# Kernel tuning notes

Hardware: AMD Instinct MI355X
Metric: run time of the kernel (lower is better)

The kernel has to match this reference:

```python
import jax, jax.numpy as jnp
import numpy as np
from jax import lax

EPOCHS = 3
N_IN, N_OUT = 20, 18
BN_EPS = 1e-5
RECT_EPS = 1e-4
TRIU = np.triu_indices(N_OUT)  # SPDVectorize upper-triangular indices


def _orth(key, n, m):
    # Stiefel init: orthonormal columns, like nn.init.orthogonal_
    q, _ = jnp.linalg.qr(jax.random.normal(key, (n, m), dtype=jnp.float32))
    return q


def setup_inputs() -> dict:
    key = jax.random.key(0)
    ks = jax.random.split(key, 8)
    bs = 2048
    f32 = jnp.float32
    return dict(
        x=jax.random.normal(ks[0], (bs, 1, 22, 438), dtype=f32),
        W1=jax.random.normal(ks[1], (22, 1, 22, 1), dtype=f32) * 0.1,
        b1=jnp.zeros((22,), f32),
        g1=jnp.ones((22,), f32), be1=jnp.zeros((22,), f32),
        W2=jax.random.normal(ks[2], (20, 22, 1, 12), dtype=f32) * 0.05,
        b2=jnp.zeros((20,), f32),
        g2=jnp.ones((20,), f32), be2=jnp.zeros((20,), f32),
        Wq=_orth(ks[3], N_IN, N_OUT),
        Wk=_orth(ks[4], N_IN, N_OUT),
        Wv=_orth(ks[5], N_IN, N_OUT),
        Wl=jax.random.normal(ks[6], (N_OUT * (N_OUT + 1) // 2 * EPOCHS, 4), dtype=f32) * 0.02,
        bl=jnp.zeros((4,), f32),
    )


def _bn(x, g, b):
    # BatchNorm2d forward in training mode (batch statistics, biased var)
    mean = x.mean(axis=(0, 2, 3), keepdims=True)
    var = ((x - mean) ** 2).mean(axis=(0, 2, 3), keepdims=True)
    return (x - mean) * lax.rsqrt(var + BN_EPS) * g[None, :, None, None] + b[None, :, None, None]


def _conv(x, w, b, pad_w):
    y = lax.conv_general_dilated(x, w, (1, 1), [(0, 0), (pad_w, pad_w)],
                                 dimension_numbers=('NCHW', 'OIHW', 'NCHW'))
    return y + b[None, :, None, None]


def _signal2spd(x):
    # x: (bs, C, L) -> trace-normalized covariance + 1e-5 * I
    L = x.shape[-1]
    xc = x - x.mean(-1, keepdims=True)
    cov = jnp.einsum('bcl,bdl->bcd', xc, xc) / (L - 1)
    cov = cov / jnp.trace(cov, axis1=-2, axis2=-1)[:, None, None]
    return cov + 1e-5 * jnp.eye(cov.shape[-1], dtype=cov.dtype)


def _patch_lens(n, epochs):
    base = n // epochs
    lens = [base] * epochs
    for i in range(n - base * epochs):
        lens[i] += 1
    return lens


def _spd_fn(t, fn):
    # SPD functional calculus via eigh (== torch.svd on SPD input)
    s, u = jnp.linalg.eigh(t)
    return jnp.einsum('...ij,...j,...kj->...ik', u, fn(s), u)


def _forward(x, W1, b1, g1, be1, W2, b2, g2, be2, Wq, Wk, Wv, Wl, bl):
    bs = x.shape[0]
    h = _bn(_conv(x, W1, b1, 0), g1, be1)          # (bs,22,1,438)
    h = _bn(_conv(h, W2, b2, 6), g2, be2)          # (bs,20,1,439)
    sig = h[:, :, 0, :]                            # squeeze -> (bs,20,439)
    covs, off = [], 0
    for L in _patch_lens(sig.shape[-1], EPOCHS):   # E2R: [147,146,146]
        covs.append(_signal2spd(sig[:, :, off:off + L]))
        off += L
    X = jnp.stack(covs, axis=1)                    # (bs,m,20,20) SPD
    # SPDTransform: W^T X W with Stiefel W (20,18)
    Q = jnp.einsum('pi,bmpq,qj->bmij', Wq, X, Wq)
    K = jnp.einsum('pi,bmpq,qj->bmij', Wk, X, Wk)
    V = jnp.einsum('pi,bmpq,qj->bmij', Wv, X, Wv)
    logQ = _spd_fn(Q, jnp.log)
    logK = _spd_fn(K, jnp.log)
    logV = _spd_fn(V, jnp.log)
    # log-Euclidean distance^2: ||log Q_j - log K_i||_F^2  (== sum of svd singvals of D D^T)
    diff = logQ[:, :, None] - logK[:, None, :]     # (bs, mq, mk, n, n)
    energy = jnp.sum(diff * diff, axis=(-2, -1))   # (bs, mq, mk)
    scores = 1.0 / (1.0 + jnp.log1p(energy))
    # torch: softmax over dim=-2 then permute(0,2,1) == softmax over K index here
    P = jax.nn.softmax(scores, axis=-1)            # (bs, mq, mk)
    mixed = jnp.einsum('bji,bipq->bjpq', P, logV)  # weighted log-Euclidean mean
    out = _spd_fn(mixed, jnp.exp)
    out = _spd_fn(out, lambda s: jnp.maximum(s, RECT_EPS))  # SPDRectified
    logO = _spd_fn(out, jnp.log)                   # SPDTangentSpace log
    vec = logO[..., TRIU[0], TRIU[1]]              # (bs, m, 171)
    return vec.reshape(bs, -1) @ Wl + bl           # (bs, 4)


def reference(x, W1, b1, g1, be1, W2, b2, g2, be2, Wq, Wk, Wv, Wl, bl):
    return _forward(x, W1, b1, g1, be1, W2, b2, g2, be2, Wq, Wk, Wv, Wl, bl)
```

## Files before the change

### kernel.cpp

```cpp
#include <hip/hip_runtime.h>
#include <math.h>

#define OFF_G3   0
#define OFF_QKV  17981440
#define OFF_ST   (17981440 + 5971968)
#define ST_SX   0
#define ST_SXX  22
#define ST_WF   506
#define ST_BF   990
#define ST_Y2S  1012
#define ST_Y2Q  1032
#define ST_TOT  1052

#define LOGEPS -9.210340371976182f
#define NSWEEP 5
#define SHIFT  12.0f

__global__ __launch_bounds__(256) void k0_zero(float* __restrict__ st){
  for (int i = threadIdx.x; i < ST_TOT; i += 256) st[i] = 0.f;
}

__global__ __launch_bounds__(256) void k1_xstats(const float* __restrict__ x, float* __restrict__ st){
  __shared__ __align__(16) float xs[22*444];
  const float* xb = x + (size_t)blockIdx.x * (22*438);
  for (int i = threadIdx.x; i < 22*444; i += 256){
    int h = i / 444, w = i - h*444;
    xs[i] = (w < 438) ? xb[h*438 + w] : 0.f;
  }
  __syncthreads();
  for (int t = threadIdx.x; t < 275; t += 256){
    if (t < 22){
      const float4* r = (const float4*)&xs[t*444];
      float4 acc = {0.f,0.f,0.f,0.f};
      for (int w = 0; w < 111; ++w){ float4 v = r[w]; acc.x+=v.x; acc.y+=v.y; acc.z+=v.z; acc.w+=v.w; }
      atomicAdd(&st[ST_SX + t], acc.x+acc.y+acc.z+acc.w);
    } else {
      int rem = t - 22, h = 0;
      while (rem >= 22 - h){ rem -= 22 - h; ++h; }
      int h2 = h + rem;
      const float4* ra = (const float4*)&xs[h*444];
      const float4* rb = (const float4*)&xs[h2*444];
      float4 acc = {0.f,0.f,0.f,0.f};
      for (int w = 0; w < 111; ++w){
        float4 a = ra[w], b = rb[w];
        acc.x = fmaf(a.x,b.x,acc.x); acc.y = fmaf(a.y,b.y,acc.y);
        acc.z = fmaf(a.z,b.z,acc.z); acc.w = fmaf(a.w,b.w,acc.w);
      }
      atomicAdd(&st[ST_SXX + h*22 + h2], acc.x+acc.y+acc.z+acc.w);
    }
  }
}

__global__ __launch_bounds__(64) void k1b_fold(const float* __restrict__ W1, const float* __restrict__ g1,
                                               const float* __restrict__ be1, float* __restrict__ st){
  int c = threadIdx.x;
  if (c >= 22) return;
  const float invN = 1.f / (2048.f*438.f);
  float mcol[22];
  float mu0 = 0.f;
  for (int h = 0; h < 22; ++h){ mcol[h] = W1[c*22 + h]; mu0 = fmaf(mcol[h], st[ST_SX + h], mu0); }
  mu0 *= invN;
  float qf = 0.f;
  for (int h = 0; h < 22; ++h)
    for (int h2 = h; h2 < 22; ++h2){
      float w = mcol[h]*mcol[h2]*st[ST_SXX + h*22 + h2];
      qf += (h2 == h) ? w : 2.f*w;
    }
  qf *= invN;
  float var = qf - mu0*mu0;
  float a1 = g1[c] * rsqrtf(var + 1e-5f);
  for (int h = 0; h < 22; ++h) st[ST_WF + h*22 + c] = a1 * mcol[h];
  st[ST_BF + c] = be1[c] - a1 * mu0;
}

__global__ __launch_bounds__(256) void k2_weff(const float* __restrict__ W2, const float* __restrict__ st,
                                               float* __restrict__ weff2, float* __restrict__ pfx){
  __shared__ float wf[484];
  __shared__ float bf[22];
  for (int i = threadIdx.x; i < 484; i += 256) wf[i] = st[ST_WF + i];
  if (threadIdx.x < 22) bf[threadIdx.x] = st[ST_BF + threadIdx.x];
  __syncthreads();
  for (int i = threadIdx.x; i < 5280; i += 256){
    int t = i % 12; int tmp = i / 12;
    int dl = tmp % 5; tmp /= 5;
    int h = tmp % 22; int dg = tmp / 22;
    int d = dg*5 + dl;
    float a = 0.f;
    for (int c = 0; c < 22; ++c) a = fmaf(W2[d*264 + c*12 + t], wf[h*22 + c], a);
    weff2[i] = a;
  }
  if (threadIdx.x < 20){
    int d = threadIdx.x;
    float run = 0.f;
    pfx[d*13 + 0] = 0.f;
    for (int t = 0; t < 12; ++t){
      float a = 0.f;
      for (int c = 0; c < 22; ++c) a = fmaf(W2[d*264 + c*12 + t], bf[c], a);
      run += a;
      pfx[d*13 + t + 1] = run;
    }
  }
}

__global__ __launch_bounds__(512, 3) void k3_convg(const float* __restrict__ x,
    const float* __restrict__ weff2, const float* __restrict__ pfx,
    float* __restrict__ st, float* __restrict__ g3o){
  __shared__ __align__(16) float smem[10304];
  float* ps   = smem + 9944;
  float* sloc = smem + 10204;
  float* qloc = smem + 10224;
  float* mus  = smem + 10244;
  int tid = threadIdx.x;
  int n = blockIdx.x;
  const float* xb = x + (size_t)n*9636;
  for (int i = tid; i < 22*452; i += 512){
    int h = i / 452, w = i - h*452;
    int gx = w - 6;
    smem[i] = (gx >= 0 && gx < 438) ? xb[h*438 + gx] : 0.f;
  }
  if (tid < 260) ps[tid] = pfx[tid];
  if (tid < 40){ if (tid < 20) sloc[tid] = 0.f; else qloc[tid-20] = 0.f; }
  __syncthreads();
  int wave = tid >> 6;
  int dg = __builtin_amdgcn_readfirstlane(wave >> 1);
  int ct = tid & 127;
  bool act = ct < 110;
  int c0 = act ? ct*4 : 0;
  float acc[5][4];
  #pragma unroll
  for (int dl = 0; dl < 5; ++dl)
    #pragma unroll
    for (int j = 0; j < 4; ++j) acc[dl][j] = 0.f;
  const float* wb = weff2 + dg*1320;
  #pragma unroll 1
  for (int h = 0; h < 22; ++h){
    const float4* xr = (const float4*)&smem[h*452 + c0];
    float4 v0 = xr[0], v1 = xr[1], v2 = xr[2], v3 = xr[3];
    float xw[16] = {v0.x,v0.y,v0.z,v0.w, v1.x,v1.y,v1.z,v1.w,
                    v2.x,v2.y,v2.z,v2.w, v3.x,v3.y,v3.z,v3.w};
    const float* wp = wb + h*60;
    #pragma unroll
    for (int dl = 0; dl < 5; ++dl){
      #pragma unroll
      for (int t = 0; t < 12; ++t){
        float w = wp[dl*12 + t];
        #pragma unroll
        for (int j = 0; j < 4; ++j)
          acc[dl][j] = fmaf(w, xw[t+j], acc[dl][j]);
      }
    }
  }
  float s5[5], q5[5];
  #pragma unroll
  for (int dl = 0; dl < 5; ++dl){ s5[dl] = 0.f; q5[dl] = 0.f; }
  if (act){
    #pragma unroll
    for (int dl = 0; dl < 5; ++dl){
      int d = dg*5 + dl;
      #pragma unroll
      for (int j = 0; j < 4; ++j){
        int gw = c0 + j;
        if (gw < 439){
          int lo = 6 - gw; if (lo < 0) lo = 0;
          int hi = 444 - gw; if (hi > 12) hi = 12;
          float val = acc[dl][j] + (ps[d*13 + hi] - ps[d*13 + lo]);
          acc[dl][j] = val;
          s5[dl] += val; q5[dl] = fmaf(val, val, q5[dl]);
        }
      }
    }
  }
  #pragma unroll
  for (int off = 32; off; off >>= 1){
    #pragma unroll
    for (int dl = 0; dl < 5; ++dl){
      s5[dl] += __shfl_down(s5[dl], off);
      q5[dl] += __shfl_down(q5[dl], off);
    }
  }
  if ((tid & 63) == 0){
    #pragma unroll
    for (int dl = 0; dl < 5; ++dl){
      atomicAdd(&sloc[dg*5 + dl], s5[dl]);
      atomicAdd(&qloc[dg*5 + dl], q5[dl]);
    }
  }
  __syncthreads();
  if (tid < 20){
    atomicAdd(&st[ST_Y2S + tid], sloc[tid]);
    atomicAdd(&st[ST_Y2Q + tid], qloc[tid]);
  }
  if (act){
    #pragma unroll
    for (int dl = 0; dl < 5; ++dl){
      int d = dg*5 + dl;
      #pragma unroll
      for (int j = 0; j < 4; ++j){
        int gw = c0 + j;
        if (gw < 439){
          int m = (gw >= 293) ? 2 : ((gw >= 147) ? 1 : 0);
          int lw = gw - ((m == 2) ? 293 : ((m == 1) ? 147 : 0));
          smem[m*2960 + d*148 + lw] = acc[dl][j];
        }
      }
    }
  }
  if (tid < 100){
    int d = tid/5, k = tid - d*5;
    int m = (k == 0) ? 0 : ((k < 3) ? 1 : 2);
    int lw = (k == 0) ? 147 : ((k == 1 || k == 3) ? 146 : 147);
    smem[m*2960 + d*148 + lw] = 0.f;
  }
  __syncthreads();
  if (tid < 60){
    int m = tid/20, d = tid - m*20;
    const float4* r = (const float4*)&smem[m*2960 + d*148];
    float4 a4 = {0.f,0.f,0.f,0.f};
    #pragma unroll 1
    for (int w = 0; w < 37; ++w){ float4 v = r[w]; a4.x+=v.x; a4.y+=v.y; a4.z+=v.z; a4.w+=v.w; }
    mus[tid] = a4.x+a4.y+a4.z+a4.w;
  }
  __syncthreads();
  for (int it = tid; it < 630; it += 512){
    int m = it/210, t = it - m*210;
    int rem = t, c = 0;
    while (rem >= 20 - c){ rem -= 20 - c; ++c; }
    int d = c + rem;
    const float4* ra = (const float4*)&smem[m*2960 + c*148];
    const float4* rb = (const float4*)&smem[m*2960 + d*148];
    float4 acc4 = {0.f,0.f,0.f,0.f};
    #pragma unroll 1
    for (int w = 0; w < 37; ++w){
      float4 a = ra[w], b = rb[w];
      acc4.x = fmaf(a.x,b.x,acc4.x); acc4.y = fmaf(a.y,b.y,acc4.y);
      acc4.z = fmaf(a.z,b.z,acc4.z); acc4.w = fmaf(a.w,b.w,acc4.w);
    }
    float invL = (m == 0) ? (1.f/147.f) : (1.f/146.f);
    float a = (acc4.x+acc4.y+acc4.z+acc4.w) - mus[m*20+c]*mus[m*20+d]*invL;
    float* gm = g3o + (size_t)n*1200 + m*400;
    gm[c*20 + d] = a; gm[d*20 + c] = a;
  }
}

__global__ __launch_bounds__(256) void k4_qkv(const float* __restrict__ g3i, const float* __restrict__ st,
    const float* __restrict__ g2, const float* __restrict__ Wq, const float* __restrict__ Wk,
    const float* __restrict__ Wv, float* __restrict__ qkv){
  __shared__ __align__(16) float G3[3][400];
  __shared__ float a2s[20];
  __shared__ __align__(16) float Bt[3][18][20];
  __shared__ __align__(16) float Tmt[3][360];
  __shared__ float rtr3[3];
  int tid = threadIdx.x, n = blockIdx.x;
  if (tid < 20){
    const float invN = 1.f/(2048.f*439.f);
    float s = st[ST_Y2S + tid]*invN;
    float q = st[ST_Y2Q + tid]*invN;
    a2s[tid] = g2[tid] * rsqrtf(q - s*s + 1e-5f);
  }
  const float* gi = g3i + (size_t)n*1200;
  for (int i = tid; i < 1200; i += 256) (&G3[0][0])[i] = gi[i];
  __syncthreads();
  for (int i = tid; i < 1080; i += 256){
    int wt = i/360, r = i - wt*360; int d = r/18, jj = r - d*18;
    const float* Wm = (wt==0) ? Wq : ((wt==1) ? Wk : Wv);
    Bt[wt][jj][d] = a2s[d]*Wm[d*18 + jj];
  }
  __syncthreads();
  for (int wt = 0; wt < 3; ++wt){
    for (int i = tid; i < 1083; i += 256){
      if (i < 1080){
        int m = i/360, r = i - m*360; int p = r/18, jj = r - p*18;
        const float4* gr = (const float4*)&G3[m][p*20];
        const float4* br = (const float4*)&Bt[wt][jj][0];
        float4 a4 = {0.f,0.f,0.f,0.f};
        #pragma unroll
        for (int w = 0; w < 5; ++w){
          float4 a = gr[w], b = br[w];
          a4.x = fmaf(a.x,b.x,a4.x); a4.y = fmaf(a.y,b.y,a4.y);
          a4.z = fmaf(a.z,b.z,a4.z); a4.w = fmaf(a.w,b.w,a4.w);
        }
        Tmt[m][jj*20 + p] = a4.x+a4.y+a4.z+a4.w;
      } else if (wt == 0){
        int m = i - 1080;
        float tr = 0.f;
        for (int c = 0; c < 20; ++c){ float a = a2s[c]; tr = fmaf(a*a, G3[m][c*21], tr); }
        rtr3[m] = 1.f/tr;
      }
    }
    __syncthreads();
    for (int it = tid; it < 513; it += 256){
      int m = it/171, t = it - m*171;
      int rem = t, i = 0;
      while (rem >= 18 - i){ rem -= 18 - i; ++i; }
      int jj = i + rem;
      const float4* br = (const float4*)&Bt[wt][i][0];
      const float4* tr = (const float4*)&Tmt[m][jj*20];
      float4 a4 = {0.f,0.f,0.f,0.f};
      #pragma unroll
      for (int w = 0; w < 5; ++w){
        float4 a = br[w], b = tr[w];
        a4.x = fmaf(a.x,b.x,a4.x); a4.y = fmaf(a.y,b.y,a4.y);
        a4.z = fmaf(a.z,b.z,a4.z); a4.w = fmaf(a.w,b.w,a4.w);
      }
      float acc = (a4.x+a4.y+a4.z+a4.w) * rtr3[m];
      if (i == jj) acc += 1e-5f;
      float* outm = qkv + ((size_t)wt*6144 + (size_t)n*3 + m)*324;
      outm[i*18 + jj] = acc; outm[jj*18 + i] = acc;
    }
    __syncthreads();
  }
}

__global__ __launch_bounds__(256, 4) void k5_oneside(const float* __restrict__ src, float* __restrict__ dst,
    int nmat, int mode, const float* __restrict__ Wl, const float* __restrict__ bl,
    float* __restrict__ outp){
  __shared__ __align__(16) float stage[12][384];
  __shared__ __align__(16) float wls[2052];
  __shared__ float outacc[4][4];
  int tid = threadIdx.x;
  int wave = tid >> 6, lane = tid & 63;
  int g = (lane >= 54) ? 3 : (lane >= 36 ? 2 : (lane >= 18 ? 1 : 0));
  int j = lane - g*18;
  int gb = g*18;
  int slot = wave*3 + ((g < 3) ? g : 0);
  int mat = blockIdx.x*12 + wave*3 + g;
  bool act = (g < 3) && (mat < nmat);

  if (mode == 1){
    for (int i = tid; i < 2052; i += 256) wls[i] = Wl[i];
    if (tid < 16) outacc[tid >> 2][tid & 3] = 0.f;
  }

  float b[18];
  float sh = (mode == 1) ? SHIFT : 0.f;
  if (act){
    const float* s = src + (size_t)mat*324 + j*18;
    #pragma unroll
    for (int i = 0; i < 18; ++i) b[i] = s[i] + ((i == j) ? sh : 0.f);
  } else {
    #pragma unroll
    for (int i = 0; i < 18; ++i) b[i] = (i == j) ? 1.f : 0.f;
  }
  float nrm;
  { float n0 = 0.f, n1 = 0.f;
    #pragma unroll
    for (int k = 0; k < 18; k += 2){ n0 = fmaf(b[k],b[k],n0); n1 = fmaf(b[k+1],b[k+1],n1); }
    nrm = n0 + n1; }

  #pragma unroll 1
  for (int sweep = 0; sweep < NSWEEP; ++sweep){
    #pragma unroll
    for (int r = 0; r < 17; ++r){
      int xx = j - 1 - r; if (xx < 0) xx += 17;
      int v = r + 17 - xx; if (v >= 17) v -= 17;
      int m = (j == 0) ? (1 + r) : ((xx == 0) ? 0 : (1 + v));
      bool isp = (j == 0) ? true : ((xx == 0) ? false : (xx <= 8));
      int plane = (gb + m) & 63;
      float rv[18];
      #pragma unroll
      for (int k = 0; k < 18; ++k) rv[k] = __shfl(b[k], plane);
      float on = __shfl(nrm, plane);
      float g0 = 0.f, g1 = 0.f;
      #pragma unroll
      for (int k = 0; k < 18; k += 2){ g0 = fmaf(b[k], rv[k], g0); g1 = fmaf(b[k+1], rv[k+1], g1); }
      float gam = g0 + g1;
      float alpha = isp ? nrm : on;
      float beta  = isp ? on  : nrm;
      float tau = (beta - alpha) * 0.5f * __builtin_amdgcn_rcpf(gam);
      float tt = __builtin_amdgcn_rcpf(fabsf(tau) + sqrtf(fmaf(tau, tau, 1.f)));
      float t = (tau >= 0.f) ? tt : -tt;
      if (!(fabsf(gam) > 1e-36f)) t = 0.f;
      float c = __builtin_amdgcn_rsqf(fmaf(t, t, 1.f));
      float s = t*c;
      nrm = fmaf(isp ? -t : t, gam, nrm);
      float sg = isp ? -s : s;
      #pragma unroll
      for (int k = 0; k < 18; ++k) b[k] = fmaf(c, b[k], sg*rv[k]);
    }
  }
  float n0 = 0.f, n1 = 0.f;
  #pragma unroll
  for (int k = 0; k < 18; k += 2){ n0 = fmaf(b[k],b[k],n0); n1 = fmaf(b[k+1],b[k+1],n1); }
  float nf = fmaxf(n0 + n1, 1e-30f);
  float fv = (mode == 0) ? (0.5f * logf(nf)) : fmaxf(sqrtf(nf) - SHIFT, LOGEPS);
  float wv = fv * __builtin_amdgcn_rcpf(nf);
  float* sp = &stage[slot][0];
  if (act){
    #pragma unroll
    for (int k = 0; k < 18; ++k) sp[k*20 + j] = b[k];
    sp[360 + j] = wv;
  }
  __syncthreads();
  if (act){
    float wr[18];
    #pragma unroll
    for (int i = 0; i < 18; ++i) wr[i] = sp[j*20 + i] * sp[360 + i];
    float frow[18];
    #pragma unroll
    for (int i2 = 0; i2 < 18; ++i2){
      const float* br = &sp[i2*20];
      float a0 = 0.f;
      #pragma unroll
      for (int k = 0; k < 16; k += 4){
        float4 v4 = *(const float4*)&br[k];
        a0 = fmaf(wr[k],   v4.x, a0); a0 = fmaf(wr[k+1], v4.y, a0);
        a0 = fmaf(wr[k+2], v4.z, a0); a0 = fmaf(wr[k+3], v4.w, a0);
      }
      a0 = fmaf(wr[16], br[16], a0);
      a0 = fmaf(wr[17], br[17], a0);
      frow[i2] = a0;
    }
    if (mode == 0){
      float* orow = dst + (size_t)mat*324 + j*18;
      #pragma unroll
      for (int i2 = 0; i2 < 18; ++i2) orow[i2] = frow[i2];
    } else {
      int base = (g*171 + j*(37 - j)/2 - j)*4;
      float o0=0.f, o1=0.f, o2=0.f, o3=0.f;
      #pragma unroll
      for (int jj = 0; jj < 18; ++jj){
        if (jj >= j){
          const float* w4 = &wls[base + jj*4];
          o0 = fmaf(frow[jj], w4[0], o0);
          o1 = fmaf(frow[jj], w4[1], o1);
          o2 = fmaf(frow[jj], w4[2], o2);
          o3 = fmaf(frow[jj], w4[3], o3);
        }
      }
      atomicAdd(&outacc[wave][0], o0);
      atomicAdd(&outacc[wave][1], o1);
      atomicAdd(&outacc[wave][2], o2);
      atomicAdd(&outacc[wave][3], o3);
    }
  }
  if (mode == 1){
    __syncthreads();
    if (tid < 16){
      int bi = tid >> 2, o = tid & 3;
      outp[(blockIdx.x*4 + bi)*4 + o] = outacc[bi][o] + bl[o];
    }
  }
}

__global__ __launch_bounds__(128) void k6_attnmix(const float* __restrict__ logs, float* __restrict__ mixed){
  __shared__ float lq[972], lk[972], lv[972];
  __shared__ float ew[2][9];
  __shared__ float P[9];
  int b = blockIdx.x, tid = threadIdx.x;
  const float* q  = logs + (size_t)b*972;
  const float* k_ = logs + 1990656 + (size_t)b*972;
  const float* v_ = logs + 3981312 + (size_t)b*972;
  for (int i = tid; i < 972; i += 128){ lq[i] = q[i]; lk[i] = k_[i]; lv[i] = v_[i]; }
  __syncthreads();
  float e[9] = {0.f,0.f,0.f,0.f,0.f,0.f,0.f,0.f,0.f};
  for (int x = tid; x < 324; x += 128){
    float q0 = lq[x], q1 = lq[324+x], q2 = lq[648+x];
    float k0 = lk[x], k1 = lk[324+x], k2 = lk[648+x];
    float d;
    d = q0-k0; e[0] = fmaf(d,d,e[0]);
    d = q0-k1; e[1] = fmaf(d,d,e[1]);
    d = q0-k2; e[2] = fmaf(d,d,e[2]);
    d = q1-k0; e[3] = fmaf(d,d,e[3]);
    d = q1-k1; e[4] = fmaf(d,d,e[4]);
    d = q1-k2; e[5] = fmaf(d,d,e[5]);
    d = q2-k0; e[6] = fmaf(d,d,e[6]);
    d = q2-k1; e[7] = fmaf(d,d,e[7]);
    d = q2-k2; e[8] = fmaf(d,d,e[8]);
  }
  #pragma unroll
  for (int p = 0; p < 9; ++p)
    for (int off = 32; off; off >>= 1) e[p] += __shfl_down(e[p], off);
  if ((tid & 63) == 0){
    #pragma unroll
    for (int p = 0; p < 9; ++p) ew[tid >> 6][p] = e[p];
  }
  __syncthreads();
  if (tid < 3){
    float en0 = ew[0][tid*3+0] + ew[1][tid*3+0];
    float en1 = ew[0][tid*3+1] + ew[1][tid*3+1];
    float en2 = ew[0][tid*3+2] + ew[1][tid*3+2];
    float s0 = 1.f/(1.f + log1pf(en0));
    float s1 = 1.f/(1.f + log1pf(en1));
    float s2 = 1.f/(1.f + log1pf(en2));
    float mx = fmaxf(s0, fmaxf(s1, s2));
    float e0 = expf(s0-mx), e1 = expf(s1-mx), e2 = expf(s2-mx);
    float inv = 1.f/(e0+e1+e2);
    P[tid*3+0] = e0*inv; P[tid*3+1] = e1*inv; P[tid*3+2] = e2*inv;
  }
  __syncthreads();
  float p00=P[0],p01=P[1],p02=P[2],p10=P[3],p11=P[4],p12=P[5],p20=P[6],p21=P[7],p22=P[8];
  float* mb = mixed + (size_t)b*972;
  for (int x = tid; x < 324; x += 128){
    float v0 = lv[x], v1 = lv[324+x], v2 = lv[648+x];
    mb[x]     = p00*v0 + p01*v1 + p02*v2;
    mb[324+x] = p10*v0 + p11*v1 + p12*v2;
    mb[648+x] = p20*v0 + p21*v1 + p22*v2;
  }
}

extern "C" void kernel_launch(void* const* d_in, const int* in_sizes, int n_in,
                              void* d_out, int out_size, void* d_ws, size_t ws_size,
                              hipStream_t stream){
  (void)in_sizes; (void)n_in; (void)out_size; (void)ws_size;
  const float* x   = (const float*)d_in[0];
  const float* W1  = (const float*)d_in[1];
  const float* g1  = (const float*)d_in[3];
  const float* be1 = (const float*)d_in[4];
  const float* W2  = (const float*)d_in[5];
  const float* g2  = (const float*)d_in[7];
  const float* Wq  = (const float*)d_in[9];
  const float* Wk  = (const float*)d_in[10];
  const float* Wv  = (const float*)d_in[11];
  const float* Wl  = (const float*)d_in[12];
  const float* bl  = (const float*)d_in[13];
  float* ws    = (float*)d_ws;
  float* g3buf = ws + OFF_G3;
  float* qkv   = ws + OFF_QKV;
  float* weff2 = ws + OFF_QKV;
  float* pfx   = ws + OFF_QKV + 5280;
  float* logs  = ws + OFF_G3;
  float* mixed = ws + OFF_QKV;
  float* st    = ws + OFF_ST;
  float* outp  = (float*)d_out;

  k0_zero    <<<dim3(1),       dim3(256), 0, stream>>>(st);
  k1_xstats  <<<dim3(2048),    dim3(256), 0, stream>>>(x, st);
  k1b_fold   <<<dim3(1),       dim3(64),  0, stream>>>(W1, g1, be1, st);
  k2_weff    <<<dim3(1),       dim3(256), 0, stream>>>(W2, st, weff2, pfx);
  k3_convg   <<<dim3(2048),    dim3(512), 0, stream>>>(x, weff2, pfx, st, g3buf);
  k4_qkv     <<<dim3(2048),    dim3(256), 0, stream>>>(g3buf, st, g2, Wq, Wk, Wv, qkv);
  k5_oneside <<<dim3(1536),    dim3(256), 0, stream>>>(qkv, logs, 18432, 0, nullptr, nullptr, nullptr);
  k6_attnmix <<<dim3(2048),    dim3(128), 0, stream>>>(logs, mixed);
  k5_oneside <<<dim3(512),     dim3(256), 0, stream>>>(mixed, nullptr, 6144, 1, Wl, bl, outp);
}
```

Baseline: 695.3 us.

## Fuse QKV projection, eigen-log and attention mix into one per-sample kernel

Merges the QKV bilinear projection, the Jacobi eigendecomposition log of the Q/K/V matrices, and the attention energy/softmax/mix into one kernel per batch sample. The 18x18 matrices stay in shared memory, so the QKV and log buffers are no longer written to and read back from global memory and two launches go away. The Jacobi sweep loop is factored into a shared device function reused by the output-stage kernel. The conv kernel also reads the prefix table straight from global memory rather than staging it in LDS, and its launch bound is raised to 8 to allow more occupancy, which may raise register pressure or cause spills.

```diff
diff --git a/kernel.cpp b/kernel.cpp
--- a/kernel.cpp
+++ b/kernel.cpp
@@ -102,14 +102,13 @@
   }
 }
 
-__global__ __launch_bounds__(512, 3) void k3_convg(const float* __restrict__ x,
+__global__ __launch_bounds__(512, 8) void k3_convg(const float* __restrict__ x,
     const float* __restrict__ weff2, const float* __restrict__ pfx,
     float* __restrict__ st, float* __restrict__ g3o){
-  __shared__ __align__(16) float smem[10304];
-  float* ps   = smem + 9944;
-  float* sloc = smem + 10204;
-  float* qloc = smem + 10224;
-  float* mus  = smem + 10244;
+  __shared__ __align__(16) float smem[10044];
+  float* sloc = smem + 9944;
+  float* qloc = smem + 9964;
+  float* mus  = smem + 9984;
   int tid = threadIdx.x;
   int n = blockIdx.x;
   const float* xb = x + (size_t)n*9636;
@@ -118,7 +117,6 @@
     int gx = w - 6;
     smem[i] = (gx >= 0 && gx < 438) ? xb[h*438 + gx] : 0.f;
   }
-  if (tid < 260) ps[tid] = pfx[tid];
   if (tid < 40){ if (tid < 20) sloc[tid] = 0.f; else qloc[tid-20] = 0.f; }
   __syncthreads();
   int wave = tid >> 6;
@@ -157,13 +155,14 @@
     #pragma unroll
     for (int dl = 0; dl < 5; ++dl){
       int d = dg*5 + dl;
+      const float* prd = pfx + d*13;
       #pragma unroll
       for (int j = 0; j < 4; ++j){
         int gw = c0 + j;
         if (gw < 439){
           int lo = 6 - gw; if (lo < 0) lo = 0;
           int hi = 444 - gw; if (hi > 12) hi = 12;
-          float val = acc[dl][j] + (ps[d*13 + hi] - ps[d*13 + lo]);
+          float val = acc[dl][j] + (prd[hi] - prd[lo]);
           acc[dl][j] = val;
           s5[dl] += val; q5[dl] = fmaf(val, val, q5[dl]);
         }
@@ -242,15 +241,56 @@
   }
 }
 
-__global__ __launch_bounds__(256) void k4_qkv(const float* __restrict__ g3i, const float* __restrict__ st,
-    const float* __restrict__ g2, const float* __restrict__ Wq, const float* __restrict__ Wk,
-    const float* __restrict__ Wv, float* __restrict__ qkv){
-  __shared__ __align__(16) float G3[3][400];
+__device__ __forceinline__ void jacobi_sweeps(float b[18], float& nrm, int j, int gb){
+  #pragma unroll 1
+  for (int sweep = 0; sweep < NSWEEP; ++sweep){
+    #pragma unroll
+    for (int r = 0; r < 17; ++r){
+      int xx = j - 1 - r; if (xx < 0) xx += 17;
+      int v = r + 17 - xx; if (v >= 17) v -= 17;
+      int m = (j == 0) ? (1 + r) : ((xx == 0) ? 0 : (1 + v));
+      bool isp = (j == 0) ? true : ((xx == 0) ? false : (xx <= 8));
+      int plane = (gb + m) & 63;
+      float rv[18];
+      #pragma unroll
+      for (int k = 0; k < 18; ++k) rv[k] = __shfl(b[k], plane);
+      float on = __shfl(nrm, plane);
+      float g0 = 0.f, g1 = 0.f;
+      #pragma unroll
+      for (int k = 0; k < 18; k += 2){ g0 = fmaf(b[k], rv[k], g0); g1 = fmaf(b[k+1], rv[k+1], g1); }
+      float gam = g0 + g1;
+      float alpha = isp ? nrm : on;
+      float beta  = isp ? on  : nrm;
+      float tau = (beta - alpha) * 0.5f * __builtin_amdgcn_rcpf(gam);
+      float tt = __builtin_amdgcn_rcpf(fabsf(tau) + sqrtf(fmaf(tau, tau, 1.f)));
+      float t = (tau >= 0.f) ? tt : -tt;
+      if (!(fabsf(gam) > 1e-36f)) t = 0.f;
+      float c = __builtin_amdgcn_rsqf(fmaf(t, t, 1.f));
+      float s = t*c;
+      nrm = fmaf(isp ? -t : t, gam, nrm);
+      float sg = isp ? -s : s;
+      #pragma unroll
+      for (int k = 0; k < 18; ++k) b[k] = fmaf(c, b[k], sg*rv[k]);
+    }
+  }
+}
+
+__global__ __launch_bounds__(192, 6) void k5_mega(const float* __restrict__ g3i,
+    const float* __restrict__ st, const float* __restrict__ g2,
+    const float* __restrict__ Wq, const float* __restrict__ Wk, const float* __restrict__ Wv,
+    float* __restrict__ mixedo){
+  __shared__ __align__(16) float S[3420];
+  __shared__ __align__(16) float L[1539];
   __shared__ float a2s[20];
-  __shared__ __align__(16) float Bt[3][18][20];
-  __shared__ __align__(16) float Tmt[3][360];
   __shared__ float rtr3[3];
+  __shared__ float ew[3][9];
+  __shared__ float P[9];
   int tid = threadIdx.x, n = blockIdx.x;
+  int wave = tid >> 6, lane = tid & 63;
+
+  float* G3s = S;
+  float* Bt  = S + 1200;
+  float* Tmt = S + 2280;
   if (tid < 20){
     const float invN = 1.f/(2048.f*439.f);
     float s = st[ST_Y2S + tid]*invN;
@@ -258,20 +298,20 @@
     a2s[tid] = g2[tid] * rsqrtf(q - s*s + 1e-5f);
   }
   const float* gi = g3i + (size_t)n*1200;
-  for (int i = tid; i < 1200; i += 256) (&G3[0][0])[i] = gi[i];
-  __syncthreads();
-  for (int i = tid; i < 1080; i += 256){
+  for (int i = tid; i < 1200; i += 192) G3s[i] = gi[i];
+  __syncthreads();
+  for (int i = tid; i < 1080; i += 192){
     int wt = i/360, r = i - wt*360; int d = r/18, jj = r - d*18;
     const float* Wm = (wt==0) ? Wq : ((wt==1) ? Wk : Wv);
-    Bt[wt][jj][d] = a2s[d]*Wm[d*18 + jj];
+    Bt[wt*360 + jj*20 + d] = a2s[d]*Wm[d*18 + jj];
   }
   __syncthreads();
   for (int wt = 0; wt < 3; ++wt){
-    for (int i = tid; i < 1083; i += 256){
+    for (int i = tid; i < 1083; i += 192){
       if (i < 1080){
         int m = i/360, r = i - m*360; int p = r/18, jj = r - p*18;
-        const float4* gr = (const float4*)&G3[m][p*20];
-        const float4* br = (const float4*)&Bt[wt][jj][0];
+        const float4* gr = (const float4*)&G3s[m*400 + p*20];
+        const float4* br = (const float4*)&Bt[wt*360 + jj*20];
         float4 a4 = {0.f,0.f,0.f,0.f};
         #pragma unroll
         for (int w = 0; w < 5; ++w){
@@ -279,22 +319,22 @@
           a4.x = fmaf(a.x,b.x,a4.x); a4.y = fmaf(a.y,b.y,a4.y);
           a4.z = fmaf(a.z,b.z,a4.z); a4.w = fmaf(a.w,b.w,a4.w);
         }
-        Tmt[m][jj*20 + p] = a4.x+a4.y+a4.z+a4.w;
+        Tmt[m*360 + jj*20 + p] = a4.x+a4.y+a4.z+a4.w;
       } else if (wt == 0){
         int m = i - 1080;
         float tr = 0.f;
-        for (int c = 0; c < 20; ++c){ float a = a2s[c]; tr = fmaf(a*a, G3[m][c*21], tr); }
+        for (int c = 0; c < 20; ++c){ float a = a2s[c]; tr = fmaf(a*a, G3s[m*400 + c*21], tr); }
         rtr3[m] = 1.f/tr;
       }
     }
     __syncthreads();
-    for (int it = tid; it < 513; it += 256){
+    for (int it = tid; it < 513; it += 192){
       int m = it/171, t = it - m*171;
       int rem = t, i = 0;
       while (rem >= 18 - i){ rem -= 18 - i; ++i; }
       int jj = i + rem;
-      const float4* br = (const float4*)&Bt[wt][i][0];
-      const float4* tr = (const float4*)&Tmt[m][jj*20];
+      const float4* br = (const float4*)&Bt[wt*360 + i*20];
+      const float4* tr = (const float4*)&Tmt[m*360 + jj*20];
       float4 a4 = {0.f,0.f,0.f,0.f};
       #pragma unroll
       for (int w = 0; w < 5; ++w){
@@ -304,10 +344,122 @@
       }
       float acc = (a4.x+a4.y+a4.z+a4.w) * rtr3[m];
       if (i == jj) acc += 1e-5f;
-      float* outm = qkv + ((size_t)wt*6144 + (size_t)n*3 + m)*324;
-      outm[i*18 + jj] = acc; outm[jj*18 + i] = acc;
+      L[(wt*3 + m)*171 + i*(35-i)/2 + jj] = acc;
     }
     __syncthreads();
+  }
+
+  int g = (lane >= 54) ? 3 : (lane >= 36 ? 2 : (lane >= 18 ? 1 : 0));
+  int j = lane - g*18;
+  int gb = g*18;
+  int slot = wave*3 + ((g < 3) ? g : 0);
+  bool act = (g < 3);
+  float b[18];
+  if (act){
+    const float* mt = &L[(wave*3 + g)*171];
+    #pragma unroll
+    for (int i = 0; i < 18; ++i){
+      int r = (i < j) ? i : j;
+      int c = (i < j) ? j : i;
+      b[i] = mt[r*(35-r)/2 + c];
+    }
+  } else {
+    #pragma unroll
+    for (int i = 0; i < 18; ++i) b[i] = (i == j) ? 1.f : 0.f;
+  }
+  float nrm;
+  { float n0 = 0.f, n1 = 0.f;
+    #pragma unroll
+    for (int k = 0; k < 18; k += 2){ n0 = fmaf(b[k],b[k],n0); n1 = fmaf(b[k+1],b[k+1],n1); }
+    nrm = n0 + n1; }
+  jacobi_sweeps(b, nrm, j, gb);
+  { float n0 = 0.f, n1 = 0.f;
+    #pragma unroll
+    for (int k = 0; k < 18; k += 2){ n0 = fmaf(b[k],b[k],n0); n1 = fmaf(b[k+1],b[k+1],n1); }
+    float nf = fmaxf(n0 + n1, 1e-30f);
+    float fv = 0.5f * logf(nf);
+    float wv = fv * __builtin_amdgcn_rcpf(nf);
+    float* sp = &S[slot*380];
+    if (act){
+      #pragma unroll
+      for (int k = 0; k < 18; ++k) sp[k*20 + j] = b[k];
+      sp[360 + j] = wv;
+    }
+    __syncthreads();
+    if (act){
+      float wr[18];
+      #pragma unroll
+      for (int i = 0; i < 18; ++i) wr[i] = sp[j*20 + i] * sp[360 + i];
+      float frow[18];
+      #pragma unroll
+      for (int i2 = 0; i2 < 18; ++i2){
+        const float* br = &sp[i2*20];
+        float a0 = 0.f;
+        #pragma unroll
+        for (int k = 0; k < 16; k += 4){
+          float4 v4 = *(const float4*)&br[k];
+          a0 = fmaf(wr[k],   v4.x, a0); a0 = fmaf(wr[k+1], v4.y, a0);
+          a0 = fmaf(wr[k+2], v4.z, a0); a0 = fmaf(wr[k+3], v4.w, a0);
+        }
+        a0 = fmaf(wr[16], br[16], a0);
+        a0 = fmaf(wr[17], br[17], a0);
+        frow[i2] = a0;
+      }
+      float* orow = &S[wave*1140 + g*324 + j*18];
+      #pragma unroll
+      for (int i2 = 0; i2 < 18; ++i2) orow[i2] = frow[i2];
+    }
+  }
+  __syncthreads();
+
+  const float* lq = &S[0];
+  const float* lk = &S[1140];
+  const float* lv = &S[2280];
+  float e[9] = {0.f,0.f,0.f,0.f,0.f,0.f,0.f,0.f,0.f};
+  for (int x = tid; x < 324; x += 192){
+    float q0 = lq[x], q1 = lq[324+x], q2 = lq[648+x];
+    float k0 = lk[x], k1 = lk[324+x], k2 = lk[648+x];
+    float d;
+    d = q0-k0; e[0] = fmaf(d,d,e[0]);
+    d = q0-k1; e[1] = fmaf(d,d,e[1]);
+    d = q0-k2; e[2] = fmaf(d,d,e[2]);
+    d = q1-k0; e[3] = fmaf(d,d,e[3]);
+    d = q1-k1; e[4] = fmaf(d,d,e[4]);
+    d = q1-k2; e[5] = fmaf(d,d,e[5]);
+    d = q2-k0; e[6] = fmaf(d,d,e[6]);
+    d = q2-k1; e[7] = fmaf(d,d,e[7]);
+    d = q2-k2; e[8] = fmaf(d,d,e[8]);
+  }
+  #pragma unroll
+  for (int p = 0; p < 9; ++p)
+    for (int off = 32; off; off >>= 1) e[p] += __shfl_down(e[p], off);
+  if (lane == 0){
+    #pragma unroll
+    for (int p = 0; p < 9; ++p) ew[wave][p] = e[p];
+  }
+  __syncthreads();
+  if (tid < 3){
+    float en0 = ew[0][tid*3+0] + ew[1][tid*3+0] + ew[2][tid*3+0];
+    float en1 = ew[0][tid*3+1] + ew[1][tid*3+1] + ew[2][tid*3+1];
+    float en2 = ew[0][tid*3+2] + ew[1][tid*3+2] + ew[2][tid*3+2];
+    float s0 = 1.f/(1.f + log1pf(en0));
+    float s1 = 1.f/(1.f + log1pf(en1));
+    float s2 = 1.f/(1.f + log1pf(en2));
+    float mx = fmaxf(s0, fmaxf(s1, s2));
+    float e0 = expf(s0-mx), e1 = expf(s1-mx), e2 = expf(s2-mx);
+    float inv = 1.f/(e0+e1+e2);
+    P[tid*3+0] = e0*inv; P[tid*3+1] = e1*inv; P[tid*3+2] = e2*inv;
+  }
+  __syncthreads();
+  {
+    float p00=P[0],p01=P[1],p02=P[2],p10=P[3],p11=P[4],p12=P[5],p20=P[6],p21=P[7],p22=P[8];
+    float* mb = mixedo + (size_t)n*972;
+    for (int x = tid; x < 324; x += 192){
+      float v0 = lv[x], v1 = lv[324+x], v2 = lv[648+x];
+      mb[x]     = p00*v0 + p01*v1 + p02*v2;
+      mb[324+x] = p10*v0 + p11*v1 + p12*v2;
+      mb[648+x] = p20*v0 + p21*v1 + p22*v2;
+    }
   }
 }
 
@@ -346,38 +498,7 @@
     #pragma unroll
     for (int k = 0; k < 18; k += 2){ n0 = fmaf(b[k],b[k],n0); n1 = fmaf(b[k+1],b[k+1],n1); }
     nrm = n0 + n1; }
-
-  #pragma unroll 1
-  for (int sweep = 0; sweep < NSWEEP; ++sweep){
-    #pragma unroll
-    for (int r = 0; r < 17; ++r){
-      int xx = j - 1 - r; if (xx < 0) xx += 17;
-      int v = r + 17 - xx; if (v >= 17) v -= 17;
-      int m = (j == 0) ? (1 + r) : ((xx == 0) ? 0 : (1 + v));
-      bool isp = (j == 0) ? true : ((xx == 0) ? false : (xx <= 8));
-      int plane = (gb + m) & 63;
-      float rv[18];
-      #pragma unroll
-      for (int k = 0; k < 18; ++k) rv[k] = __shfl(b[k], plane);
-      float on = __shfl(nrm, plane);
-      float g0 = 0.f, g1 = 0.f;
-      #pragma unroll
-      for (int k = 0; k < 18; k += 2){ g0 = fmaf(b[k], rv[k], g0); g1 = fmaf(b[k+1], rv[k+1], g1); }
-      float gam = g0 + g1;
-      float alpha = isp ? nrm : on;
-      float beta  = isp ? on  : nrm;
-      float tau = (beta - alpha) * 0.5f * __builtin_amdgcn_rcpf(gam);
-      float tt = __builtin_amdgcn_rcpf(fabsf(tau) + sqrtf(fmaf(tau, tau, 1.f)));
-      float t = (tau >= 0.f) ? tt : -tt;
-      if (!(fabsf(gam) > 1e-36f)) t = 0.f;
-      float c = __builtin_amdgcn_rsqf(fmaf(t, t, 1.f));
-      float s = t*c;
-      nrm = fmaf(isp ? -t : t, gam, nrm);
-      float sg = isp ? -s : s;
-      #pragma unroll
-      for (int k = 0; k < 18; ++k) b[k] = fmaf(c, b[k], sg*rv[k]);
-    }
-  }
+  jacobi_sweeps(b, nrm, j, gb);
   float n0 = 0.f, n1 = 0.f;
   #pragma unroll
   for (int k = 0; k < 18; k += 2){ n0 = fmaf(b[k],b[k],n0); n1 = fmaf(b[k+1],b[k+1],n1); }
@@ -439,62 +560,6 @@
       int bi = tid >> 2, o = tid & 3;
       outp[(blockIdx.x*4 + bi)*4 + o] = outacc[bi][o] + bl[o];
     }
-  }
-}
-
-__global__ __launch_bounds__(128) void k6_attnmix(const float* __restrict__ logs, float* __restrict__ mixed){
-  __shared__ float lq[972], lk[972], lv[972];
-  __shared__ float ew[2][9];
-  __shared__ float P[9];
-  int b = blockIdx.x, tid = threadIdx.x;
-  const float* q  = logs + (size_t)b*972;
-  const float* k_ = logs + 1990656 + (size_t)b*972;
-  const float* v_ = logs + 3981312 + (size_t)b*972;
-  for (int i = tid; i < 972; i += 128){ lq[i] = q[i]; lk[i] = k_[i]; lv[i] = v_[i]; }
-  __syncthreads();
-  float e[9] = {0.f,0.f,0.f,0.f,0.f,0.f,0.f,0.f,0.f};
-  for (int x = tid; x < 324; x += 128){
-    float q0 = lq[x], q1 = lq[324+x], q2 = lq[648+x];
-    float k0 = lk[x], k1 = lk[324+x], k2 = lk[648+x];
-    float d;
-    d = q0-k0; e[0] = fmaf(d,d,e[0]);
-    d = q0-k1; e[1] = fmaf(d,d,e[1]);
-    d = q0-k2; e[2] = fmaf(d,d,e[2]);
-    d = q1-k0; e[3] = fmaf(d,d,e[3]);
-    d = q1-k1; e[4] = fmaf(d,d,e[4]);
-    d = q1-k2; e[5] = fmaf(d,d,e[5]);
-    d = q2-k0; e[6] = fmaf(d,d,e[6]);
-    d = q2-k1; e[7] = fmaf(d,d,e[7]);
-    d = q2-k2; e[8] = fmaf(d,d,e[8]);
-  }
-  #pragma unroll
-  for (int p = 0; p < 9; ++p)
-    for (int off = 32; off; off >>= 1) e[p] += __shfl_down(e[p], off);
-  if ((tid & 63) == 0){
-    #pragma unroll
-    for (int p = 0; p < 9; ++p) ew[tid >> 6][p] = e[p];
-  }
-  __syncthreads();
-  if (tid < 3){
-    float en0 = ew[0][tid*3+0] + ew[1][tid*3+0];
-    float en1 = ew[0][tid*3+1] + ew[1][tid*3+1];
-    float en2 = ew[0][tid*3+2] + ew[1][tid*3+2];
-    float s0 = 1.f/(1.f + log1pf(en0));
-    float s1 = 1.f/(1.f + log1pf(en1));
-    float s2 = 1.f/(1.f + log1pf(en2));
-    float mx = fmaxf(s0, fmaxf(s1, s2));
-    float e0 = expf(s0-mx), e1 = expf(s1-mx), e2 = expf(s2-mx);
-    float inv = 1.f/(e0+e1+e2);
-    P[tid*3+0] = e0*inv; P[tid*3+1] = e1*inv; P[tid*3+2] = e2*inv;
-  }
-  __syncthreads();
-  float p00=P[0],p01=P[1],p02=P[2],p10=P[3],p11=P[4],p12=P[5],p20=P[6],p21=P[7],p22=P[8];
-  float* mb = mixed + (size_t)b*972;
-  for (int x = tid; x < 324; x += 128){
-    float v0 = lv[x], v1 = lv[324+x], v2 = lv[648+x];
-    mb[x]     = p00*v0 + p01*v1 + p02*v2;
-    mb[324+x] = p10*v0 + p11*v1 + p12*v2;
-    mb[648+x] = p20*v0 + p21*v1 + p22*v2;
   }
 }
 
@@ -515,21 +580,17 @@
   const float* bl  = (const float*)d_in[13];
   float* ws    = (float*)d_ws;
   float* g3buf = ws + OFF_G3;
-  float* qkv   = ws + OFF_QKV;
   float* weff2 = ws + OFF_QKV;
   float* pfx   = ws + OFF_QKV + 5280;
-  float* logs  = ws + OFF_G3;
   float* mixed = ws + OFF_QKV;
   float* st    = ws + OFF_ST;
   float* outp  = (float*)d_out;
 
-  k0_zero    <<<dim3(1),       dim3(256), 0, stream>>>(st);
-  k1_xstats  <<<dim3(2048),    dim3(256), 0, stream>>>(x, st);
-  k1b_fold   <<<dim3(1),       dim3(64),  0, stream>>>(W1, g1, be1, st);
-  k2_weff    <<<dim3(1),       dim3(256), 0, stream>>>(W2, st, weff2, pfx);
-  k3_convg   <<<dim3(2048),    dim3(512), 0, stream>>>(x, weff2, pfx, st, g3buf);
-  k4_qkv     <<<dim3(2048),    dim3(256), 0, stream>>>(g3buf, st, g2, Wq, Wk, Wv, qkv);
-  k5_oneside <<<dim3(1536),    dim3(256), 0, stream>>>(qkv, logs, 18432, 0, nullptr, nullptr, nullptr);
-  k6_attnmix <<<dim3(2048),    dim3(128), 0, stream>>>(logs, mixed);
-  k5_oneside <<<dim3(512),     dim3(256), 0, stream>>>(mixed, nullptr, 6144, 1, Wl, bl, outp);
-}
+  k0_zero    <<<dim3(1),    dim3(256), 0, stream>>>(st);
+  k1_xstats  <<<dim3(2048), dim3(256), 0, stream>>>(x, st);
+  k1b_fold   <<<dim3(1),    dim3(64),  0, stream>>>(W1, g1, be1, st);
+  k2_weff    <<<dim3(1),    dim3(256), 0, stream>>>(W2, st, weff2, pfx);
+  k3_convg   <<<dim3(2048), dim3(512), 0, stream>>>(x, weff2, pfx, st, g3buf);
+  k5_mega    <<<dim3(2048), dim3(192), 0, stream>>>(g3buf, st, g2, Wq, Wk, Wv, mixed);
+  k5_oneside <<<dim3(512),  dim3(256), 0, stream>>>(mixed, nullptr, 6144, 1, Wl, bl, outp);
+}
```

Measured after the change: 679.8 us. -2.2%, faster.
